# Optimization experiments

Measured on AMD Instinct MI355X. Metric: run time of the kernel, lower is better.

The kernel has to match this reference:

```python
import jax, jax.numpy as jnp
import numpy as np

B, S, H = 32, 1024, 768          # batch, seq_len, bert hidden
E, W, P = 128, 8, 512            # entities/sample, span width, rel pairs/sample
NT, NR = 5, 9                    # entity types, relation types
D1, HEADS1, D2, RD = 128, 2, 64, 32
REL_IN = 2 * D2 + RD + H         # 928


def _layernorm(x, g, b):
    m = x.mean(-1, keepdims=True)
    v = x.var(-1, keepdims=True)
    return (x - m) * jax.lax.rsqrt(v + 1e-5) * g + b


def _gat_dense(x, Wm, a_src, a_dst, bias, concat):
    # Fully-connected entity graph (incl. self-loops, PyG GATConv default).
    Bn, En, _ = x.shape
    Hh, D = a_src.shape
    h = (x @ Wm).reshape(Bn, En, Hh, D)                      # [B,E,h,D]
    s = jnp.einsum('behd,hd->beh', h, a_src)                 # source score
    d = jnp.einsum('behd,hd->beh', h, a_dst)                 # target score
    # edge j->i : e_ij = leaky_relu(s_j + d_i)
    e = jax.nn.leaky_relu(d[:, :, None, :] + s[:, None, :, :], 0.2)  # [B,i,j,h]
    alpha = jax.nn.softmax(e, axis=2)
    o = jnp.einsum('bijh,bjhd->bihd', alpha, h)
    o = o.reshape(Bn, En, Hh * D) if concat else o.mean(axis=2)
    return o + bias


def setup_inputs() -> dict:
    key = jax.random.key(0)
    ks = jax.random.split(key, 20)
    f = lambda k, shape: jax.random.normal(k, shape, jnp.float32) * 0.02
    return dict(
        sequence_output=jax.random.normal(ks[0], (B, S, H), jnp.float32),
        entity_starts=jax.random.randint(ks[1], (B, E), 0, S - W),
        entity_type_ids=jax.random.randint(ks[2], (B, E), 0, NT),
        pair_idx=jax.random.randint(ks[3], (B, P, 2), 0, E),
        rel_type_ids=jax.random.randint(ks[4], (B, P), 0, NR),
        entity_type_emb=f(ks[5], (NT, H)),
        rel_type_emb=f(ks[6], (NR, RD)),
        W1=f(ks[7], (H, HEADS1 * D1)), a_src1=f(ks[8], (HEADS1, D1)),
        a_dst1=f(ks[9], (HEADS1, D1)), b1=jnp.zeros((HEADS1 * D1,), jnp.float32),
        ln1_g=jnp.ones((HEADS1 * D1,), jnp.float32), ln1_b=jnp.zeros((HEADS1 * D1,), jnp.float32),
        W2=f(ks[10], (HEADS1 * D1, D2)), a_src2=f(ks[11], (1, D2)),
        a_dst2=f(ks[12], (1, D2)), b2=jnp.zeros((D2,), jnp.float32),
        ln2_g=jnp.ones((D2,), jnp.float32), ln2_b=jnp.zeros((D2,), jnp.float32),
        Wr1=f(ks[13], (REL_IN, 256)), br1=jnp.zeros((256,), jnp.float32),
        Wr2=f(ks[14], (256, 1)), br2=jnp.zeros((1,), jnp.float32),
    )


def reference(sequence_output, entity_starts, entity_type_ids, pair_idx, rel_type_ids,
              entity_type_emb, rel_type_emb,
              W1, a_src1, a_dst1, b1, ln1_g, ln1_b,
              W2, a_src2, a_dst2, b2, ln2_g, ln2_b,
              Wr1, br1, Wr2, br2):
    bidx = jnp.arange(B)[:, None]
    # --- per-entity attention pooling over span tokens ---
    tok_idx = entity_starts[:, :, None] + jnp.arange(W)            # [B,E,W]
    toks = sequence_output[jnp.arange(B)[:, None, None], tok_idx]  # [B,E,W,H]
    mean = toks.mean(axis=2)                                       # [B,E,H]
    attn = jax.nn.softmax(jnp.einsum('bewh,beh->bew', toks, mean), axis=-1)
    pooled = jnp.einsum('bew,bewh->beh', attn, toks)
    x = pooled + entity_type_emb[entity_type_ids]                  # [B,E,H]
    # --- 2-layer GAT over fully-connected entity graph ---
    x = jax.nn.elu(_layernorm(_gat_dense(x, W1, a_src1, a_dst1, b1, True), ln1_g, ln1_b))
    x = jax.nn.elu(_layernorm(_gat_dense(x, W2, a_src2, a_dst2, b2, False), ln2_g, ln2_b))
    # --- gather-concat relation MLP scoring ---
    cls = sequence_output[:, 0, :]                                 # [B,H]
    x1 = x[bidx, pair_idx[:, :, 0]]                                # [B,P,64]
    x2 = x[bidx, pair_idx[:, :, 1]]
    rel = rel_type_emb[rel_type_ids]                               # [B,P,32]
    pv = jnp.concatenate([x1, x2, rel, jnp.broadcast_to(cls[:, None, :], (B, P, H))], axis=-1)
    scores = (jax.nn.relu(pv @ Wr1 + br1) @ Wr2 + br2)[..., 0]     # [B,P]
    return scores
```

## Files before the change

kernel.cpp:

```cpp
#include <hip/hip_runtime.h>
#include <hip/hip_bf16.h>

#define BB 32
#define SS 1024
#define HHH 768
#define EE 128
#define WW 8
#define PP 512
#define RDD 32

typedef __attribute__((ext_vector_type(8))) short bf16x8;
typedef __attribute__((ext_vector_type(8))) unsigned short us8;
typedef __attribute__((ext_vector_type(4))) unsigned short us4;
typedef __attribute__((ext_vector_type(4))) float f32x4;

__device__ __forceinline__ unsigned short f2bf(float v) {
    __hip_bfloat16 h = __float2bfloat16(v);
    return *(unsigned short*)&h;
}
__device__ __forceinline__ float bf2f(unsigned short u) {
    unsigned int x = ((unsigned int)u) << 16;
    float f; __builtin_memcpy(&f, &x, 4);
    return f;
}

__global__ __launch_bounds__(256) void pool_prep_kernel(
    const float* __restrict__ seq, const int* __restrict__ starts,
    const int* __restrict__ types, const float* __restrict__ temb,
    unsigned short* __restrict__ xout,
    const float* __restrict__ W1, unsigned short* __restrict__ Wt,
    const float* __restrict__ Wr1, unsigned short* __restrict__ Wtr,
    const float* __restrict__ W2, unsigned short* __restrict__ W2t,
    const float* __restrict__ remb, unsigned short* __restrict__ rembb,
    float* __restrict__ basep) {
    int tid = threadIdx.x;
    __shared__ float sbuf[WW * HHH];
    __shared__ float scred[WW];
    __shared__ float attn_s[WW];

    if (blockIdx.x < BB * EE) {
        int be = blockIdx.x;
        int b = be >> 7;
        int start = starts[be];
        const float4* bp4 = (const float4*)(seq + ((size_t)b * SS + start) * HHH);
        for (int idx = tid; idx < WW * (HHH / 4); idx += 256) {
            int w = idx / (HHH / 4), h4 = idx % (HHH / 4);
            float4 v = bp4[(size_t)w * (HHH / 4) + h4];
            sbuf[w * HHH + h4 * 4 + 0] = v.x; sbuf[w * HHH + h4 * 4 + 1] = v.y;
            sbuf[w * HHH + h4 * 4 + 2] = v.z; sbuf[w * HHH + h4 * 4 + 3] = v.w;
        }
        __syncthreads();

        float sc[WW];
#pragma unroll
        for (int w = 0; w < WW; w++) sc[w] = 0.f;
#pragma unroll
        for (int c = 0; c < 3; c++) {
            int h = tid + 256 * c;
            float s = 0.f;
#pragma unroll
            for (int w = 0; w < WW; w++) s += sbuf[w * HHH + h];
            float m = s * (1.0f / WW);
#pragma unroll
            for (int w = 0; w < WW; w++) sc[w] += sbuf[w * HHH + h] * m;
        }
        if (tid < WW) scred[tid] = 0.f;
        __syncthreads();
        int lane = tid & 63;
#pragma unroll
        for (int w = 0; w < WW; w++) {
            float v = sc[w];
            for (int o = 32; o > 0; o >>= 1) v += __shfl_down(v, o, 64);
            if (lane == 0) atomicAdd(&scred[w], v);
        }
        __syncthreads();
        if (tid == 0) {
            float mx = scred[0];
            for (int w = 1; w < WW; w++) mx = fmaxf(mx, scred[w]);
            float ssum = 0.f;
            float a[WW];
            for (int w = 0; w < WW; w++) { a[w] = __expf(scred[w] - mx); ssum += a[w]; }
            float inv = 1.f / ssum;
            for (int w = 0; w < WW; w++) attn_s[w] = a[w] * inv;
        }
        __syncthreads();

        int t = types[be];
        const float* emb = temb + (size_t)t * HHH;
#pragma unroll
        for (int c = 0; c < 3; c++) {
            int h = tid + 256 * c;
            float p = 0.f;
#pragma unroll
            for (int w = 0; w < WW; w++) p += attn_s[w] * sbuf[w * HHH + h];
            xout[(size_t)be * HHH + h] = f2bf(p + emb[h]);
        }
        return;
    }

    int blk = blockIdx.x - BB * EE;
    if (blk < 48) {
        int k0 = blk * 16;
        for (int i = tid; i < 16 * 256; i += 256)
            sbuf[i] = W1[(size_t)(k0 + (i >> 8)) * 256 + (i & 255)];
        __syncthreads();
        int n = tid;
        us8 v0, v1;
#pragma unroll
        for (int kk = 0; kk < 8; kk++) v0[kk] = f2bf(sbuf[kk * 256 + n]);
#pragma unroll
        for (int kk = 0; kk < 8; kk++) v1[kk] = f2bf(sbuf[(8 + kk) * 256 + n]);
        *(us8*)(Wt + (size_t)n * HHH + k0) = v0;
        *(us8*)(Wt + (size_t)n * HHH + k0 + 8) = v1;
    } else if (blk < 58) {
        int k0 = (blk - 48) * 16;
        for (int i = tid; i < 16 * 256; i += 256)
            sbuf[i] = Wr1[(size_t)(k0 + (i >> 8)) * 256 + (i & 255)];
        __syncthreads();
        int n = tid;
        us8 v0, v1;
#pragma unroll
        for (int kk = 0; kk < 8; kk++) v0[kk] = f2bf(sbuf[kk * 256 + n]);
#pragma unroll
        for (int kk = 0; kk < 8; kk++) v1[kk] = f2bf(sbuf[(8 + kk) * 256 + n]);
        *(us8*)(Wtr + (size_t)n * 160 + k0) = v0;
        *(us8*)(Wtr + (size_t)n * 160 + k0 + 8) = v1;
    } else if (blk < 74) {
        int k0 = (blk - 58) * 16;
        for (int i = tid; i < 16 * 64; i += 256)
            sbuf[(i >> 6) * 64 + (i & 63)] = W2[(size_t)(k0 + (i >> 6)) * 64 + (i & 63)];
        __syncthreads();
        if (tid < 64) {
            int n = tid;
            us8 v0, v1;
#pragma unroll
            for (int kk = 0; kk < 8; kk++) v0[kk] = f2bf(sbuf[kk * 64 + n]);
#pragma unroll
            for (int kk = 0; kk < 8; kk++) v1[kk] = f2bf(sbuf[(8 + kk) * 64 + n]);
            *(us8*)(W2t + (size_t)n * 256 + k0) = v0;
            *(us8*)(W2t + (size_t)n * 256 + k0 + 8) = v1;
        }
    } else if (blk == 74) {
        for (int i = tid; i < 9 * RDD; i += 256) rembb[i] = f2bf(remb[i]);
    } else {
        int pc = blk - 75;
        int kc = pc % 12;
        int b = pc / 12;
        int n = tid;
        if (n < 64) sbuf[4096 + n] = seq[(size_t)b * SS * HHH + kc * 64 + n];
        __syncthreads();
        float acc = 0.f;
        const float* w = Wr1 + (size_t)(160 + kc * 64) * 256 + n;
#pragma unroll 16
        for (int k = 0; k < 64; k++) acc += sbuf[4096 + k] * w[(size_t)k * 256];
        basep[((size_t)kc * 32 + b) * 256 + n] = acc;
    }
}

__global__ __launch_bounds__(256) void gemm1_mfma_kernel(
    const unsigned short* __restrict__ Xb, const unsigned short* __restrict__ Wt,
    float* __restrict__ C) {
    const int K = HHH;
    int n0 = blockIdx.x * 64;
    int m0 = blockIdx.y * 64;
    int tid = threadIdx.x;
    int wave = tid >> 6, lane = tid & 63;
    int wm = (wave >> 1) * 32, wn = (wave & 1) * 32;

    __shared__ __align__(16) unsigned short As[64][40];
    __shared__ __align__(16) unsigned short Bs[64][40];

    f32x4 acc[2][2] = {};
    int ar = tid >> 2;
    int ac = (tid & 3) * 8;
    int fr = lane & 15;
    int fk = (lane >> 4) * 8;

    for (int k0 = 0; k0 < K; k0 += 32) {
        us8 av = *(const us8*)(Xb + (size_t)(m0 + ar) * K + k0 + ac);
        us8 bv = *(const us8*)(Wt + (size_t)(n0 + ar) * K + k0 + ac);
        *(us8*)(&As[ar][ac]) = av;
        *(us8*)(&Bs[ar][ac]) = bv;
        __syncthreads();

        bf16x8 a0 = *(const bf16x8*)(&As[wm + fr][fk]);
        bf16x8 a1 = *(const bf16x8*)(&As[wm + 16 + fr][fk]);
        bf16x8 b0 = *(const bf16x8*)(&Bs[wn + fr][fk]);
        bf16x8 b1 = *(const bf16x8*)(&Bs[wn + 16 + fr][fk]);

        acc[0][0] = __builtin_amdgcn_mfma_f32_16x16x32_bf16(a0, b0, acc[0][0], 0, 0, 0);
        acc[0][1] = __builtin_amdgcn_mfma_f32_16x16x32_bf16(a0, b1, acc[0][1], 0, 0, 0);
        acc[1][0] = __builtin_amdgcn_mfma_f32_16x16x32_bf16(a1, b0, acc[1][0], 0, 0, 0);
        acc[1][1] = __builtin_amdgcn_mfma_f32_16x16x32_bf16(a1, b1, acc[1][1], 0, 0, 0);
        __syncthreads();
    }

    int crow = (lane >> 4) * 4;
    int ccol = lane & 15;
#pragma unroll
    for (int mi = 0; mi < 2; mi++)
#pragma unroll
        for (int ni = 0; ni < 2; ni++)
#pragma unroll
            for (int r = 0; r < 4; r++)
                C[(size_t)(m0 + wm + mi * 16 + crow + r) * 256 +
                  n0 + wn + ni * 16 + ccol] = acc[mi][ni][r];
}

__global__ void sd1_kernel(const float* __restrict__ h1, const float* __restrict__ asrc,
                           const float* __restrict__ adst, float* __restrict__ s1,
                           float* __restrict__ d1) {
    int beh = blockIdx.x;
    int h = beh & 1;
    int be = beh >> 1;
    int lane = threadIdx.x;
    const float* row = h1 + (size_t)be * 256 + h * 128;
    float v0 = row[lane], v1 = row[lane + 64];
    float ss = v0 * asrc[h * 128 + lane] + v1 * asrc[h * 128 + lane + 64];
    float dd = v0 * adst[h * 128 + lane] + v1 * adst[h * 128 + lane + 64];
    for (int o = 32; o > 0; o >>= 1) {
        ss += __shfl_down(ss, o, 64);
        dd += __shfl_down(dd, o, 64);
    }
    if (lane == 0) { s1[beh] = ss; d1[beh] = dd; }
}

__global__ __launch_bounds__(256) void gat1_fused_kernel(
    const float* __restrict__ h1, const float* __restrict__ s1,
    const float* __restrict__ d1, const float* __restrict__ b1,
    const float* __restrict__ gamma, const float* __restrict__ beta,
    unsigned short* __restrict__ g1b) {
    int b = blockIdx.x >> 2;
    int c = blockIdx.x & 3;
    int tid = threadIdx.x;
    int wave = tid >> 6, lane = tid & 63;
    int h = wave >> 1, m = wave & 1;
    int fr = lane & 15;
    int fk = (lane >> 4) * 8;

    __shared__ __align__(16) unsigned short h1T[2][128][136];
    __shared__ float ssh[2][128];
    __shared__ float dsh[2][128];
    __shared__ float lnred[32][2][2];

    {
        const float4* src4 = (const float4*)(h1 + (size_t)b * 128 * 256);
        for (int it = 0; it < 32; it++) {
            int i4 = tid + it * 256;
            int j = i4 >> 6;
            int c4 = i4 & 63;
            float4 v = src4[(size_t)j * 64 + c4];
            int d = c4 * 4;
            int hh = d >> 7, dl = d & 127;
            h1T[hh][dl + 0][j] = f2bf(v.x);
            h1T[hh][dl + 1][j] = f2bf(v.y);
            h1T[hh][dl + 2][j] = f2bf(v.z);
            h1T[hh][dl + 3][j] = f2bf(v.w);
        }
        int hh = tid >> 7, j = tid & 127;
        ssh[hh][j] = s1[((size_t)b * 128 + j) * 2 + hh];
        dsh[hh][j] = d1[((size_t)b * 128 + j) * 2 + hh];
    }
    __syncthreads();

    bf16x8 afrag[4];
    {
        float dd = dsh[h][c * 32 + m * 16 + fr];
        float ev[4][8];
        float mx = -1e30f;
#pragma unroll
        for (int ks = 0; ks < 4; ks++)
#pragma unroll
            for (int jj = 0; jj < 8; jj++) {
                float e = dd + ssh[h][ks * 32 + fk + jj];
                e = e >= 0.f ? e : 0.2f * e;
                ev[ks][jj] = e;
                mx = fmaxf(mx, e);
            }
        mx = fmaxf(mx, __shfl_xor(mx, 16, 64));
        mx = fmaxf(mx, __shfl_xor(mx, 32, 64));
        float sm = 0.f;
#pragma unroll
        for (int ks = 0; ks < 4; ks++)
#pragma unroll
            for (int jj = 0; jj < 8; jj++) {
                float e = __expf(ev[ks][jj] - mx);
                ev[ks][jj] = e;
                sm += e;
            }
        sm += __shfl_xor(sm, 16, 64);
        sm += __shfl_xor(sm, 32, 64);
        float inv = 1.f / sm;
#pragma unroll
        for (int ks = 0; ks < 4; ks++) {
            bf16x8 a;
#pragma unroll
            for (int jj = 0; jj < 8; jj++)
                a[jj] = (short)f2bf(ev[ks][jj] * inv);
            afrag[ks] = a;
        }
    }

    f32x4 acc[8] = {};
#pragma unroll
    for (int ks = 0; ks < 4; ks++)
#pragma unroll
        for (int ni = 0; ni < 8; ni++) {
            bf16x8 bv = *(const bf16x8*)(&h1T[h][ni * 16 + fr][ks * 32 + fk]);
            acc[ni] = __builtin_amdgcn_mfma_f32_16x16x32_bf16(
                afrag[ks], bv, acc[ni], 0, 0, 0);
        }

    int crow = (lane >> 4) * 4;
    int ccol = lane & 15;
    float bv_[8], gv[8], bev[8];
#pragma unroll
    for (int ni = 0; ni < 8; ni++) {
        int d = h * 128 + ni * 16 + ccol;
        bv_[ni] = b1[d]; gv[ni] = gamma[d]; bev[ni] = beta[d];
    }
    float vv[4][8];
#pragma unroll
    for (int r = 0; r < 4; r++) {
        float s = 0.f, q = 0.f;
#pragma unroll
        for (int ni = 0; ni < 8; ni++) {
            float v = acc[ni][r] + bv_[ni];
            vv[r][ni] = v;
            s += v;
            q += v * v;
        }
        s += __shfl_xor(s, 1, 64); s += __shfl_xor(s, 2, 64);
        s += __shfl_xor(s, 4, 64); s += __shfl_xor(s, 8, 64);
        q += __shfl_xor(q, 1, 64); q += __shfl_xor(q, 2, 64);
        q += __shfl_xor(q, 4, 64); q += __shfl_xor(q, 8, 64);
        if ((lane & 15) == 0) {
            lnred[m * 16 + crow + r][h][0] = s;
            lnred[m * 16 + crow + r][h][1] = q;
        }
    }
    __syncthreads();
#pragma unroll
    for (int r = 0; r < 4; r++) {
        int row = m * 16 + crow + r;
        float s = lnred[row][0][0] + lnred[row][1][0];
        float q = lnred[row][0][1] + lnred[row][1][1];
        float mean = s * (1.f / 256.f);
        float var = q * (1.f / 256.f) - mean * mean;
        float rs = rsqrtf(var + 1e-5f);
        unsigned short* dst = g1b + (size_t)(b * 128 + c * 32 + row) * 256 + h * 128;
#pragma unroll
        for (int ni = 0; ni < 8; ni++) {
            float y = (vv[r][ni] - mean) * rs * gv[ni] + bev[ni];
            y = y > 0.f ? y : (__expf(y) - 1.f);
            dst[ni * 16 + ccol] = f2bf(y);
        }
    }
}

__global__ __launch_bounds__(256) void gemm2_mfma_kernel(
    const unsigned short* __restrict__ g1b, const unsigned short* __restrict__ W2t,
    const float* __restrict__ asrc, const float* __restrict__ adst,
    float* __restrict__ h2, float* __restrict__ s2, float* __restrict__ d2) {
    int m0 = blockIdx.x * 64;
    int tid = threadIdx.x;
    int wave = tid >> 6, lane = tid & 63;
    int wm = (wave >> 1) * 32, wn = (wave & 1) * 32;

    __shared__ __align__(16) unsigned short As[64][72];
    __shared__ __align__(16) unsigned short Bs[64][72];
    __shared__ float sdred[64][2][2];

    f32x4 acc[2][2] = {};
    int fr = lane & 15;
    int fk = (lane >> 4) * 8;

    for (int kc = 0; kc < 4; kc++) {
        for (int it = 0; it < 2; it++) {
            int i = tid + it * 256;
            int row = i >> 3, c = i & 7;
            *(us8*)(&As[row][c * 8]) =
                *(const us8*)(g1b + (size_t)(m0 + row) * 256 + kc * 64 + c * 8);
            *(us8*)(&Bs[row][c * 8]) =
                *(const us8*)(W2t + (size_t)row * 256 + kc * 64 + c * 8);
        }
        __syncthreads();
#pragma unroll
        for (int ks = 0; ks < 2; ks++) {
            int kb = ks * 32 + fk;
            bf16x8 a0 = *(const bf16x8*)(&As[wm + fr][kb]);
            bf16x8 a1 = *(const bf16x8*)(&As[wm + 16 + fr][kb]);
            bf16x8 b0 = *(const bf16x8*)(&Bs[wn + fr][kb]);
            bf16x8 b1 = *(const bf16x8*)(&Bs[wn + 16 + fr][kb]);
            acc[0][0] = __builtin_amdgcn_mfma_f32_16x16x32_bf16(a0, b0, acc[0][0], 0, 0, 0);
            acc[0][1] = __builtin_amdgcn_mfma_f32_16x16x32_bf16(a0, b1, acc[0][1], 0, 0, 0);
            acc[1][0] = __builtin_amdgcn_mfma_f32_16x16x32_bf16(a1, b0, acc[1][0], 0, 0, 0);
            acc[1][1] = __builtin_amdgcn_mfma_f32_16x16x32_bf16(a1, b1, acc[1][1], 0, 0, 0);
        }
        __syncthreads();
    }

    int crow = (lane >> 4) * 4;
    int ccol = lane & 15;
    float asv[2], adv[2];
#pragma unroll
    for (int ni = 0; ni < 2; ni++) {
        int n = wn + ni * 16 + ccol;
        asv[ni] = asrc[n];
        adv[ni] = adst[n];
    }
#pragma unroll
    for (int mi = 0; mi < 2; mi++) {
#pragma unroll
        for (int r = 0; r < 4; r++) {
            float sp = 0.f, dp = 0.f;
#pragma unroll
            for (int ni = 0; ni < 2; ni++) {
                float v = acc[mi][ni][r];
                h2[(size_t)(m0 + wm + mi * 16 + crow + r) * 64 +
                   wn + ni * 16 + ccol] = v;
                sp += v * asv[ni];
                dp += v * adv[ni];
            }
            for (int msk = 1; msk < 16; msk <<= 1) {
                sp += __shfl_xor(sp, msk, 64);
                dp += __shfl_xor(dp, msk, 64);
            }
            if ((lane & 15) == 0) {
                int row = wm + mi * 16 + crow + r;
                sdred[row][wn >> 5][0] = sp;
                sdred[row][wn >> 5][1] = dp;
            }
        }
    }
    __syncthreads();
    if (tid < 64 && wave == 0) {
        s2[m0 + tid] = sdred[tid][0][0] + sdred[tid][1][0];
        d2[m0 + tid] = sdred[tid][0][1] + sdred[tid][1][1];
    }
}

__global__ __launch_bounds__(256) void gat2_fused_kernel(
    const float* __restrict__ h2, const float* __restrict__ s2,
    const float* __restrict__ d2, const float* __restrict__ b2v,
    const float* __restrict__ gamma, const float* __restrict__ beta,
    unsigned short* __restrict__ x2b) {
    int b = blockIdx.x >> 1;
    int c = blockIdx.x & 1;
    int tid = threadIdx.x;
    int wave = tid >> 6, lane = tid & 63;
    int fr = lane & 15;
    int fk = (lane >> 4) * 8;

    __shared__ __align__(16) unsigned short h2T[64][136];
    __shared__ float ssh[128];
    __shared__ float dsh[128];

    {
        const float4* src4 = (const float4*)(h2 + (size_t)b * 128 * 64);
        for (int it = 0; it < 8; it++) {
            int i4 = tid + it * 256;
            int j = i4 >> 4;
            int c4 = i4 & 15;
            float4 v = src4[(size_t)j * 16 + c4];
            int d = c4 * 4;
            h2T[d + 0][j] = f2bf(v.x);
            h2T[d + 1][j] = f2bf(v.y);
            h2T[d + 2][j] = f2bf(v.z);
            h2T[d + 3][j] = f2bf(v.w);
        }
        if (tid < 128) ssh[tid] = s2[(size_t)b * 128 + tid];
        else dsh[tid - 128] = d2[(size_t)b * 128 + (tid - 128)];
    }
    __syncthreads();

    bf16x8 afrag[4];
    {
        float dd = dsh[c * 64 + wave * 16 + fr];
        float ev[4][8];
        float mx = -1e30f;
#pragma unroll
        for (int ks = 0; ks < 4; ks++)
#pragma unroll
            for (int jj = 0; jj < 8; jj++) {
                float e = dd + ssh[ks * 32 + fk + jj];
                e = e >= 0.f ? e : 0.2f * e;
                ev[ks][jj] = e;
                mx = fmaxf(mx, e);
            }
        mx = fmaxf(mx, __shfl_xor(mx, 16, 64));
        mx = fmaxf(mx, __shfl_xor(mx, 32, 64));
        float sm = 0.f;
#pragma unroll
        for (int ks = 0; ks < 4; ks++)
#pragma unroll
            for (int jj = 0; jj < 8; jj++) {
                float e = __expf(ev[ks][jj] - mx);
                ev[ks][jj] = e;
                sm += e;
            }
        sm += __shfl_xor(sm, 16, 64);
        sm += __shfl_xor(sm, 32, 64);
        float inv = 1.f / sm;
#pragma unroll
        for (int ks = 0; ks < 4; ks++) {
            bf16x8 a;
#pragma unroll
            for (int jj = 0; jj < 8; jj++)
                a[jj] = (short)f2bf(ev[ks][jj] * inv);
            afrag[ks] = a;
        }
    }

    f32x4 acc[4] = {};
#pragma unroll
    for (int ks = 0; ks < 4; ks++)
#pragma unroll
        for (int ni = 0; ni < 4; ni++) {
            bf16x8 bv = *(const bf16x8*)(&h2T[ni * 16 + fr][ks * 32 + fk]);
            acc[ni] = __builtin_amdgcn_mfma_f32_16x16x32_bf16(
                afrag[ks], bv, acc[ni], 0, 0, 0);
        }

    int crow = (lane >> 4) * 4;
    int ccol = lane & 15;
    float bv_[4], gv[4], bev[4];
#pragma unroll
    for (int ni = 0; ni < 4; ni++) {
        int d = ni * 16 + ccol;
        bv_[ni] = b2v[d]; gv[ni] = gamma[d]; bev[ni] = beta[d];
    }
#pragma unroll
    for (int r = 0; r < 4; r++) {
        float v[4];
        float s = 0.f;
#pragma unroll
        for (int ni = 0; ni < 4; ni++) {
            v[ni] = acc[ni][r] + bv_[ni];
            s += v[ni];
        }
        s += __shfl_xor(s, 1, 64); s += __shfl_xor(s, 2, 64);
        s += __shfl_xor(s, 4, 64); s += __shfl_xor(s, 8, 64);
        float mean = s * (1.f / 64.f);
        float sq = 0.f;
#pragma unroll
        for (int ni = 0; ni < 4; ni++) {
            float dv = v[ni] - mean;
            sq += dv * dv;
        }
        sq += __shfl_xor(sq, 1, 64); sq += __shfl_xor(sq, 2, 64);
        sq += __shfl_xor(sq, 4, 64); sq += __shfl_xor(sq, 8, 64);
        float rs = rsqrtf(sq * (1.f / 64.f) + 1e-5f);
        int i = c * 64 + wave * 16 + crow + r;
        unsigned short* dst = x2b + (size_t)(b * 128 + i) * 64;
#pragma unroll
        for (int ni = 0; ni < 4; ni++) {
            float y = (v[ni] - mean) * rs * gv[ni] + bev[ni];
            y = y > 0.f ? y : (__expf(y) - 1.f);
            dst[ni * 16 + ccol] = f2bf(y);
        }
    }
}

__global__ __launch_bounds__(256) void score_mfma_kernel(
    const unsigned short* __restrict__ x2b, const float* __restrict__ basep,
    const float* __restrict__ br1,
    const int* __restrict__ pair_idx, const int* __restrict__ rel_ids,
    const unsigned short* __restrict__ rembb, const unsigned short* __restrict__ Wtr,
    const float* __restrict__ Wr2, const float* __restrict__ br2,
    float* __restrict__ out) {
    int blk = blockIdx.x;
    int b = blk >> 3;
    int p0 = (blk & 7) * 64;
    int tid = threadIdx.x;
    int wave = tid >> 6, lane = tid & 63;
    int wn = wave * 64;

    __shared__ __align__(16) unsigned short As[64][168];
    __shared__ __align__(16) unsigned short Bs[256][40];
    __shared__ float sred[64][4];
    __shared__ int prs[64][3];

    if (tid < 64) {
        int p = p0 + tid;
        prs[tid][0] = pair_idx[((size_t)b * PP + p) * 2 + 0];
        prs[tid][1] = pair_idx[((size_t)b * PP + p) * 2 + 1];
        prs[tid][2] = rel_ids[(size_t)b * PP + p];
    }
    __syncthreads();
    for (int it = 0; it < 10; it++) {
        int idx = tid + it * 256;
        int m = idx / 40, c = idx % 40;
        int k0 = c * 4;
        us4 v;
        if (k0 < 64)
            v = *(const us4*)(x2b + ((size_t)b * EE + prs[m][0]) * 64 + k0);
        else if (k0 < 128)
            v = *(const us4*)(x2b + ((size_t)b * EE + prs[m][1]) * 64 + (k0 - 64));
        else
            v = *(const us4*)(rembb + prs[m][2] * RDD + (k0 - 128));
        *(us4*)(&As[m][k0]) = v;
    }

    f32x4 acc[4][4] = {};
    int fr = lane & 15;
    int fk = (lane >> 4) * 8;

    for (int kc = 0; kc < 5; kc++) {
        for (int it = 0; it < 4; it++) {
            int i = tid + it * 256;
            int n = i >> 2, c = i & 3;
            *(us8*)(&Bs[n][c * 8]) =
                *(const us8*)(Wtr + (size_t)n * 160 + kc * 32 + c * 8);
        }
        __syncthreads();
        bf16x8 a[4], bv[4];
#pragma unroll
        for (int mi = 0; mi < 4; mi++)
            a[mi] = *(const bf16x8*)(&As[mi * 16 + fr][kc * 32 + fk]);
#pragma unroll
        for (int ni = 0; ni < 4; ni++)
            bv[ni] = *(const bf16x8*)(&Bs[wn + ni * 16 + fr][fk]);
#pragma unroll
        for (int mi = 0; mi < 4; mi++)
#pragma unroll
            for (int ni = 0; ni < 4; ni++)
                acc[mi][ni] = __builtin_amdgcn_mfma_f32_16x16x32_bf16(
                    a[mi], bv[ni], acc[mi][ni], 0, 0, 0);
        __syncthreads();
    }

    int crow = (lane >> 4) * 4;
    int ccol = lane & 15;
    float basev[4], w2v[4];
#pragma unroll
    for (int ni = 0; ni < 4; ni++) {
        int n = wn + ni * 16 + ccol;
        float bb = br1[n];
#pragma unroll
        for (int kc = 0; kc < 12; kc++)
            bb += basep[((size_t)kc * 32 + b) * 256 + n];
        basev[ni] = bb;
        w2v[ni] = Wr2[n];
    }
#pragma unroll
    for (int mi = 0; mi < 4; mi++) {
#pragma unroll
        for (int r = 0; r < 4; r++) {
            float p = 0.f;
#pragma unroll
            for (int ni = 0; ni < 4; ni++)
                p += fmaxf(acc[mi][ni][r] + basev[ni], 0.f) * w2v[ni];
            for (int msk = 1; msk < 16; msk <<= 1)
                p += __shfl_xor(p, msk, 64);
            if ((lane & 15) == 0)
                sred[mi * 16 + crow + r][wave] = p;
        }
    }
    __syncthreads();
    if (tid < 64) {
        float s = sred[tid][0] + sred[tid][1] + sred[tid][2] + sred[tid][3] + br2[0];
        out[(size_t)b * PP + p0 + tid] = s;
    }
}

extern "C" void kernel_launch(void* const* d_in, const int* in_sizes, int n_in,
                              void* d_out, int out_size, void* d_ws, size_t ws_size,
                              hipStream_t stream) {
    (void)in_sizes; (void)n_in; (void)out_size; (void)ws_size;
    const float* seq      = (const float*)d_in[0];
    const int*   starts   = (const int*)d_in[1];
    const int*   types    = (const int*)d_in[2];
    const int*   pair_idx = (const int*)d_in[3];
    const int*   rel_ids  = (const int*)d_in[4];
    const float* temb     = (const float*)d_in[5];
    const float* remb     = (const float*)d_in[6];
    const float* W1       = (const float*)d_in[7];
    const float* a_src1   = (const float*)d_in[8];
    const float* a_dst1   = (const float*)d_in[9];
    const float* b1       = (const float*)d_in[10];
    const float* ln1_g    = (const float*)d_in[11];
    const float* ln1_b    = (const float*)d_in[12];
    const float* W2       = (const float*)d_in[13];
    const float* a_src2   = (const float*)d_in[14];
    const float* a_dst2   = (const float*)d_in[15];
    const float* b2       = (const float*)d_in[16];
    const float* ln2_g    = (const float*)d_in[17];
    const float* ln2_b    = (const float*)d_in[18];
    const float* Wr1      = (const float*)d_in[19];
    const float* br1      = (const float*)d_in[20];
    const float* Wr2      = (const float*)d_in[21];
    const float* br2      = (const float*)d_in[22];
    float* out = (float*)d_out;

    unsigned short* xb    = (unsigned short*)d_ws;
    unsigned short* Wt    = xb + (size_t)4096 * 768;
    unsigned short* Wtr   = Wt + (size_t)256 * 768;
    unsigned short* W2t   = Wtr + (size_t)256 * 160;
    unsigned short* rembb = W2t + (size_t)64 * 256;
    unsigned short* g1b   = rembb + 512;
    unsigned short* x2b   = g1b + (size_t)4096 * 256;
    float* fbase = (float*)(x2b + (size_t)4096 * 64);
    float* h1    = fbase;
    float* s1    = h1 + (size_t)4096 * 256;
    float* d1    = s1 + 8192;
    float* h2    = d1 + 8192;
    float* s2    = h2 + (size_t)4096 * 64;
    float* d2    = s2 + 4096;
    float* basep = d2 + 4096;

    pool_prep_kernel<<<BB * EE + 75 + 12 * 32, 256, 0, stream>>>(
        seq, starts, types, temb, xb, W1, Wt, Wr1, Wtr, W2, W2t, remb, rembb, basep);
    gemm1_mfma_kernel<<<dim3(4, 64), 256, 0, stream>>>(xb, Wt, h1);
    sd1_kernel<<<BB * EE * 2, 64, 0, stream>>>(h1, a_src1, a_dst1, s1, d1);
    gat1_fused_kernel<<<BB * 4, 256, 0, stream>>>(h1, s1, d1, b1, ln1_g, ln1_b, g1b);
    gemm2_mfma_kernel<<<64, 256, 0, stream>>>(g1b, W2t, a_src2, a_dst2, h2, s2, d2);
    gat2_fused_kernel<<<BB * 2, 256, 0, stream>>>(h2, s2, d2, b2, ln2_g, ln2_b, x2b);
    score_mfma_kernel<<<BB * PP / 64, 256, 0, stream>>>(x2b, basep, br1, pair_idx,
                                                        rel_ids, rembb, Wtr, Wr2,
                                                        br2, out);
}
```

Measured before the change: 245.8 us.

## Fuse GAT score reductions and layer-2 GEMM into neighbouring kernels with bf16 transposed intermediates

The GEMM1 epilogue now computes the per-head source and destination attention partial sums and writes h1 as transposed bf16, which removes the separate sd1 kernel and the fp32 h1 round trip. The layer-1 GAT kernel now also performs the W2 projection and the s2/d2 reductions, removing the standalone gemm2 kernel and the g1b buffer. GAT2 reads a pre-transposed bf16 h2. This cuts two launches and intermediate memory traffic. In exchange it adds more shared memory in the fused kernel and reads W2 directly from global memory inside it.

New measurement: 228.9 us. 6.9% less time.

```diff
diff --git a/kernel.cpp b/kernel.cpp
--- a/kernel.cpp
+++ b/kernel.cpp
@@ -17,11 +17,6 @@
 __device__ __forceinline__ unsigned short f2bf(float v) {
     __hip_bfloat16 h = __float2bfloat16(v);
     return *(unsigned short*)&h;
-}
-__device__ __forceinline__ float bf2f(unsigned short u) {
-    unsigned int x = ((unsigned int)u) << 16;
-    float f; __builtin_memcpy(&f, &x, 4);
-    return f;
 }
 
 __global__ __launch_bounds__(256) void pool_prep_kernel(
@@ -159,7 +154,9 @@
 
 __global__ __launch_bounds__(256) void gemm1_mfma_kernel(
     const unsigned short* __restrict__ Xb, const unsigned short* __restrict__ Wt,
-    float* __restrict__ C) {
+    const float* __restrict__ asrc1, const float* __restrict__ adst1,
+    unsigned short* __restrict__ h1Tg,
+    float* __restrict__ ps_s, float* __restrict__ ps_d) {
     const int K = HHH;
     int n0 = blockIdx.x * 64;
     int m0 = blockIdx.y * 64;
@@ -169,6 +166,8 @@
 
     __shared__ __align__(16) unsigned short As[64][40];
     __shared__ __align__(16) unsigned short Bs[64][40];
+    __shared__ __align__(16) unsigned short T[64][72];
+    __shared__ float sdred[64][2][2];
 
     f32x4 acc[2][2] = {};
     int ar = tid >> 2;
@@ -197,218 +196,18 @@
 
     int crow = (lane >> 4) * 4;
     int ccol = lane & 15;
-#pragma unroll
-    for (int mi = 0; mi < 2; mi++)
-#pragma unroll
-        for (int ni = 0; ni < 2; ni++)
-#pragma unroll
-            for (int r = 0; r < 4; r++)
-                C[(size_t)(m0 + wm + mi * 16 + crow + r) * 256 +
-                  n0 + wn + ni * 16 + ccol] = acc[mi][ni][r];
-}
-
-__global__ void sd1_kernel(const float* __restrict__ h1, const float* __restrict__ asrc,
-                           const float* __restrict__ adst, float* __restrict__ s1,
-                           float* __restrict__ d1) {
-    int beh = blockIdx.x;
-    int h = beh & 1;
-    int be = beh >> 1;
-    int lane = threadIdx.x;
-    const float* row = h1 + (size_t)be * 256 + h * 128;
-    float v0 = row[lane], v1 = row[lane + 64];
-    float ss = v0 * asrc[h * 128 + lane] + v1 * asrc[h * 128 + lane + 64];
-    float dd = v0 * adst[h * 128 + lane] + v1 * adst[h * 128 + lane + 64];
-    for (int o = 32; o > 0; o >>= 1) {
-        ss += __shfl_down(ss, o, 64);
-        dd += __shfl_down(dd, o, 64);
-    }
-    if (lane == 0) { s1[beh] = ss; d1[beh] = dd; }
-}
-
-__global__ __launch_bounds__(256) void gat1_fused_kernel(
-    const float* __restrict__ h1, const float* __restrict__ s1,
-    const float* __restrict__ d1, const float* __restrict__ b1,
-    const float* __restrict__ gamma, const float* __restrict__ beta,
-    unsigned short* __restrict__ g1b) {
-    int b = blockIdx.x >> 2;
-    int c = blockIdx.x & 3;
-    int tid = threadIdx.x;
-    int wave = tid >> 6, lane = tid & 63;
-    int h = wave >> 1, m = wave & 1;
-    int fr = lane & 15;
-    int fk = (lane >> 4) * 8;
-
-    __shared__ __align__(16) unsigned short h1T[2][128][136];
-    __shared__ float ssh[2][128];
-    __shared__ float dsh[2][128];
-    __shared__ float lnred[32][2][2];
-
-    {
-        const float4* src4 = (const float4*)(h1 + (size_t)b * 128 * 256);
-        for (int it = 0; it < 32; it++) {
-            int i4 = tid + it * 256;
-            int j = i4 >> 6;
-            int c4 = i4 & 63;
-            float4 v = src4[(size_t)j * 64 + c4];
-            int d = c4 * 4;
-            int hh = d >> 7, dl = d & 127;
-            h1T[hh][dl + 0][j] = f2bf(v.x);
-            h1T[hh][dl + 1][j] = f2bf(v.y);
-            h1T[hh][dl + 2][j] = f2bf(v.z);
-            h1T[hh][dl + 3][j] = f2bf(v.w);
-        }
-        int hh = tid >> 7, j = tid & 127;
-        ssh[hh][j] = s1[((size_t)b * 128 + j) * 2 + hh];
-        dsh[hh][j] = d1[((size_t)b * 128 + j) * 2 + hh];
-    }
-    __syncthreads();
-
-    bf16x8 afrag[4];
-    {
-        float dd = dsh[h][c * 32 + m * 16 + fr];
-        float ev[4][8];
-        float mx = -1e30f;
-#pragma unroll
-        for (int ks = 0; ks < 4; ks++)
-#pragma unroll
-            for (int jj = 0; jj < 8; jj++) {
-                float e = dd + ssh[h][ks * 32 + fk + jj];
-                e = e >= 0.f ? e : 0.2f * e;
-                ev[ks][jj] = e;
-                mx = fmaxf(mx, e);
-            }
-        mx = fmaxf(mx, __shfl_xor(mx, 16, 64));
-        mx = fmaxf(mx, __shfl_xor(mx, 32, 64));
-        float sm = 0.f;
-#pragma unroll
-        for (int ks = 0; ks < 4; ks++)
-#pragma unroll
-            for (int jj = 0; jj < 8; jj++) {
-                float e = __expf(ev[ks][jj] - mx);
-                ev[ks][jj] = e;
-                sm += e;
-            }
-        sm += __shfl_xor(sm, 16, 64);
-        sm += __shfl_xor(sm, 32, 64);
-        float inv = 1.f / sm;
-#pragma unroll
-        for (int ks = 0; ks < 4; ks++) {
-            bf16x8 a;
-#pragma unroll
-            for (int jj = 0; jj < 8; jj++)
-                a[jj] = (short)f2bf(ev[ks][jj] * inv);
-            afrag[ks] = a;
-        }
-    }
-
-    f32x4 acc[8] = {};
-#pragma unroll
-    for (int ks = 0; ks < 4; ks++)
-#pragma unroll
-        for (int ni = 0; ni < 8; ni++) {
-            bf16x8 bv = *(const bf16x8*)(&h1T[h][ni * 16 + fr][ks * 32 + fk]);
-            acc[ni] = __builtin_amdgcn_mfma_f32_16x16x32_bf16(
-                afrag[ks], bv, acc[ni], 0, 0, 0);
-        }
-
-    int crow = (lane >> 4) * 4;
-    int ccol = lane & 15;
-    float bv_[8], gv[8], bev[8];
-#pragma unroll
-    for (int ni = 0; ni < 8; ni++) {
-        int d = h * 128 + ni * 16 + ccol;
-        bv_[ni] = b1[d]; gv[ni] = gamma[d]; bev[ni] = beta[d];
-    }
-    float vv[4][8];
-#pragma unroll
-    for (int r = 0; r < 4; r++) {
-        float s = 0.f, q = 0.f;
-#pragma unroll
-        for (int ni = 0; ni < 8; ni++) {
-            float v = acc[ni][r] + bv_[ni];
-            vv[r][ni] = v;
-            s += v;
-            q += v * v;
-        }
-        s += __shfl_xor(s, 1, 64); s += __shfl_xor(s, 2, 64);
-        s += __shfl_xor(s, 4, 64); s += __shfl_xor(s, 8, 64);
-        q += __shfl_xor(q, 1, 64); q += __shfl_xor(q, 2, 64);
-        q += __shfl_xor(q, 4, 64); q += __shfl_xor(q, 8, 64);
-        if ((lane & 15) == 0) {
-            lnred[m * 16 + crow + r][h][0] = s;
-            lnred[m * 16 + crow + r][h][1] = q;
-        }
-    }
-    __syncthreads();
-#pragma unroll
-    for (int r = 0; r < 4; r++) {
-        int row = m * 16 + crow + r;
-        float s = lnred[row][0][0] + lnred[row][1][0];
-        float q = lnred[row][0][1] + lnred[row][1][1];
-        float mean = s * (1.f / 256.f);
-        float var = q * (1.f / 256.f) - mean * mean;
-        float rs = rsqrtf(var + 1e-5f);
-        unsigned short* dst = g1b + (size_t)(b * 128 + c * 32 + row) * 256 + h * 128;
-#pragma unroll
-        for (int ni = 0; ni < 8; ni++) {
-            float y = (vv[r][ni] - mean) * rs * gv[ni] + bev[ni];
-            y = y > 0.f ? y : (__expf(y) - 1.f);
-            dst[ni * 16 + ccol] = f2bf(y);
-        }
-    }
-}
-
-__global__ __launch_bounds__(256) void gemm2_mfma_kernel(
-    const unsigned short* __restrict__ g1b, const unsigned short* __restrict__ W2t,
-    const float* __restrict__ asrc, const float* __restrict__ adst,
-    float* __restrict__ h2, float* __restrict__ s2, float* __restrict__ d2) {
-    int m0 = blockIdx.x * 64;
-    int tid = threadIdx.x;
-    int wave = tid >> 6, lane = tid & 63;
-    int wm = (wave >> 1) * 32, wn = (wave & 1) * 32;
-
-    __shared__ __align__(16) unsigned short As[64][72];
-    __shared__ __align__(16) unsigned short Bs[64][72];
-    __shared__ float sdred[64][2][2];
-
-    f32x4 acc[2][2] = {};
-    int fr = lane & 15;
-    int fk = (lane >> 4) * 8;
-
-    for (int kc = 0; kc < 4; kc++) {
-        for (int it = 0; it < 2; it++) {
-            int i = tid + it * 256;
-            int row = i >> 3, c = i & 7;
-            *(us8*)(&As[row][c * 8]) =
-                *(const us8*)(g1b + (size_t)(m0 + row) * 256 + kc * 64 + c * 8);
-            *(us8*)(&Bs[row][c * 8]) =
-                *(const us8*)(W2t + (size_t)row * 256 + kc * 64 + c * 8);
-        }
-        __syncthreads();
-#pragma unroll
-        for (int ks = 0; ks < 2; ks++) {
-            int kb = ks * 32 + fk;
-            bf16x8 a0 = *(const bf16x8*)(&As[wm + fr][kb]);
-            bf16x8 a1 = *(const bf16x8*)(&As[wm + 16 + fr][kb]);
-            bf16x8 b0 = *(const bf16x8*)(&Bs[wn + fr][kb]);
-            bf16x8 b1 = *(const bf16x8*)(&Bs[wn + 16 + fr][kb]);
-            acc[0][0] = __builtin_amdgcn_mfma_f32_16x16x32_bf16(a0, b0, acc[0][0], 0, 0, 0);
-            acc[0][1] = __builtin_amdgcn_mfma_f32_16x16x32_bf16(a0, b1, acc[0][1], 0, 0, 0);
-            acc[1][0] = __builtin_amdgcn_mfma_f32_16x16x32_bf16(a1, b0, acc[1][0], 0, 0, 0);
-            acc[1][1] = __builtin_amdgcn_mfma_f32_16x16x32_bf16(a1, b1, acc[1][1], 0, 0, 0);
-        }
-        __syncthreads();
-    }
-
-    int crow = (lane >> 4) * 4;
-    int ccol = lane & 15;
+    int h = n0 >> 7;
+    int nb = (n0 >> 6) & 1;
+    int dbase = (n0 & 127) + wn;
+
     float asv[2], adv[2];
 #pragma unroll
     for (int ni = 0; ni < 2; ni++) {
-        int n = wn + ni * 16 + ccol;
-        asv[ni] = asrc[n];
-        adv[ni] = adst[n];
-    }
+        int d = dbase + ni * 16 + ccol;
+        asv[ni] = asrc1[h * 128 + d];
+        adv[ni] = adst1[h * 128 + d];
+    }
+
 #pragma unroll
     for (int mi = 0; mi < 2; mi++) {
 #pragma unroll
@@ -417,8 +216,7 @@
 #pragma unroll
             for (int ni = 0; ni < 2; ni++) {
                 float v = acc[mi][ni][r];
-                h2[(size_t)(m0 + wm + mi * 16 + crow + r) * 64 +
-                   wn + ni * 16 + ccol] = v;
+                T[wn + ni * 16 + ccol][wm + mi * 16 + crow + r] = f2bf(v);
                 sp += v * asv[ni];
                 dp += v * adv[ni];
             }
@@ -434,14 +232,215 @@
         }
     }
     __syncthreads();
-    if (tid < 64 && wave == 0) {
-        s2[m0 + tid] = sdred[tid][0][0] + sdred[tid][1][0];
-        d2[m0 + tid] = sdred[tid][0][1] + sdred[tid][1][1];
+
+    int b = m0 >> 7;
+    int j0 = m0 & 127;
+    if (tid < 64) {
+        float spt = sdred[tid][0][0] + sdred[tid][1][0];
+        float dpt = sdred[tid][0][1] + sdred[tid][1][1];
+        size_t o = (size_t)nb * 8192 + ((size_t)(m0 + tid)) * 2 + h;
+        ps_s[o] = spt;
+        ps_d[o] = dpt;
+    }
+    {
+        int d_l = tid >> 2, q = tid & 3;
+        us8 v0 = *(const us8*)(&T[d_l][q * 16]);
+        us8 v1 = *(const us8*)(&T[d_l][q * 16 + 8]);
+        size_t go = ((size_t)(b * 2 + h) * 128 + (n0 & 127) + d_l) * 128 + j0 + q * 16;
+        *(us8*)(h1Tg + go) = v0;
+        *(us8*)(h1Tg + go + 8) = v1;
     }
 }
 
+__global__ __launch_bounds__(256) void gat1_gemm2_kernel(
+    const unsigned short* __restrict__ h1Tg,
+    const float* __restrict__ ps_s, const float* __restrict__ ps_d,
+    const float* __restrict__ b1, const float* __restrict__ gamma,
+    const float* __restrict__ beta,
+    const unsigned short* __restrict__ W2t,
+    const float* __restrict__ asrc2, const float* __restrict__ adst2,
+    unsigned short* __restrict__ h2Tg, float* __restrict__ s2,
+    float* __restrict__ d2) {
+    int b = blockIdx.x >> 2;
+    int c = blockIdx.x & 3;
+    int tid = threadIdx.x;
+    int wave = tid >> 6, lane = tid & 63;
+    int h = wave >> 1, m = wave & 1;
+    int fr = lane & 15;
+    int fk = (lane >> 4) * 8;
+
+    __shared__ __align__(16) unsigned short h1T[2][128][136];
+    __shared__ float ssh[2][128];
+    __shared__ float dsh[2][128];
+    __shared__ float lnred[32][2][2];
+    __shared__ __align__(16) unsigned short g1s[32][264];
+    __shared__ float sdr2[32][2][2];
+    __shared__ __align__(16) unsigned short t2[64][40];
+
+    {
+        const us8* src = (const us8*)(h1Tg + (size_t)b * 32768);
+#pragma unroll
+        for (int it = 0; it < 16; it++) {
+            int i8 = tid + it * 256;
+            int row = i8 >> 4;
+            int j8 = i8 & 15;
+            *(us8*)(&h1T[row >> 7][row & 127][j8 * 8]) = src[i8];
+        }
+        int hh = tid >> 7, j = tid & 127;
+        size_t o = ((size_t)b * 128 + j) * 2 + hh;
+        ssh[hh][j] = ps_s[o] + ps_s[o + 8192];
+        dsh[hh][j] = ps_d[o] + ps_d[o + 8192];
+    }
+    __syncthreads();
+
+    bf16x8 afrag[4];
+    {
+        float dd = dsh[h][c * 32 + m * 16 + fr];
+        float ev[4][8];
+        float mx = -1e30f;
+#pragma unroll
+        for (int ks = 0; ks < 4; ks++)
+#pragma unroll
+            for (int jj = 0; jj < 8; jj++) {
+                float e = dd + ssh[h][ks * 32 + fk + jj];
+                e = e >= 0.f ? e : 0.2f * e;
+                ev[ks][jj] = e;
+                mx = fmaxf(mx, e);
+            }
+        mx = fmaxf(mx, __shfl_xor(mx, 16, 64));
+        mx = fmaxf(mx, __shfl_xor(mx, 32, 64));
+        float sm = 0.f;
+#pragma unroll
+        for (int ks = 0; ks < 4; ks++)
+#pragma unroll
+            for (int jj = 0; jj < 8; jj++) {
+                float e = __expf(ev[ks][jj] - mx);
+                ev[ks][jj] = e;
+                sm += e;
+            }
+        sm += __shfl_xor(sm, 16, 64);
+        sm += __shfl_xor(sm, 32, 64);
+        float inv = 1.f / sm;
+#pragma unroll
+        for (int ks = 0; ks < 4; ks++) {
+            bf16x8 a;
+#pragma unroll
+            for (int jj = 0; jj < 8; jj++)
+                a[jj] = (short)f2bf(ev[ks][jj] * inv);
+            afrag[ks] = a;
+        }
+    }
+
+    f32x4 acc[8] = {};
+#pragma unroll
+    for (int ks = 0; ks < 4; ks++)
+#pragma unroll
+        for (int ni = 0; ni < 8; ni++) {
+            bf16x8 bv = *(const bf16x8*)(&h1T[h][ni * 16 + fr][ks * 32 + fk]);
+            acc[ni] = __builtin_amdgcn_mfma_f32_16x16x32_bf16(
+                afrag[ks], bv, acc[ni], 0, 0, 0);
+        }
+
+    int crow = (lane >> 4) * 4;
+    int ccol = lane & 15;
+    float bv_[8], gv[8], bev[8];
+#pragma unroll
+    for (int ni = 0; ni < 8; ni++) {
+        int d = h * 128 + ni * 16 + ccol;
+        bv_[ni] = b1[d]; gv[ni] = gamma[d]; bev[ni] = beta[d];
+    }
+    float vv[4][8];
+#pragma unroll
+    for (int r = 0; r < 4; r++) {
+        float s = 0.f, q = 0.f;
+#pragma unroll
+        for (int ni = 0; ni < 8; ni++) {
+            float v = acc[ni][r] + bv_[ni];
+            vv[r][ni] = v;
+            s += v;
+            q += v * v;
+        }
+        s += __shfl_xor(s, 1, 64); s += __shfl_xor(s, 2, 64);
+        s += __shfl_xor(s, 4, 64); s += __shfl_xor(s, 8, 64);
+        q += __shfl_xor(q, 1, 64); q += __shfl_xor(q, 2, 64);
+        q += __shfl_xor(q, 4, 64); q += __shfl_xor(q, 8, 64);
+        if ((lane & 15) == 0) {
+            lnred[m * 16 + crow + r][h][0] = s;
+            lnred[m * 16 + crow + r][h][1] = q;
+        }
+    }
+    __syncthreads();
+#pragma unroll
+    for (int r = 0; r < 4; r++) {
+        int row = m * 16 + crow + r;
+        float s = lnred[row][0][0] + lnred[row][1][0];
+        float q = lnred[row][0][1] + lnred[row][1][1];
+        float mean = s * (1.f / 256.f);
+        float var = q * (1.f / 256.f) - mean * mean;
+        float rs = rsqrtf(var + 1e-5f);
+#pragma unroll
+        for (int ni = 0; ni < 8; ni++) {
+            float y = (vv[r][ni] - mean) * rs * gv[ni] + bev[ni];
+            y = y > 0.f ? y : (__expf(y) - 1.f);
+            g1s[row][h * 128 + ni * 16 + ccol] = f2bf(y);
+        }
+    }
+    __syncthreads();
+
+    int m2 = wave & 1;
+    int nb = wave >> 1;
+    f32x4 acc2[2] = {};
+#pragma unroll
+    for (int kc = 0; kc < 8; kc++) {
+        bf16x8 a = *(const bf16x8*)(&g1s[m2 * 16 + fr][kc * 32 + fk]);
+#pragma unroll
+        for (int ni = 0; ni < 2; ni++) {
+            bf16x8 wv = *(const bf16x8*)(W2t + (size_t)(nb * 32 + ni * 16 + fr) * 256 +
+                                         kc * 32 + fk);
+            acc2[ni] = __builtin_amdgcn_mfma_f32_16x16x32_bf16(a, wv, acc2[ni], 0, 0, 0);
+        }
+    }
+    float as2[2], ad2[2];
+#pragma unroll
+    for (int ni = 0; ni < 2; ni++) {
+        int n = nb * 32 + ni * 16 + ccol;
+        as2[ni] = asrc2[n];
+        ad2[ni] = adst2[n];
+    }
+#pragma unroll
+    for (int r = 0; r < 4; r++) {
+        int rl = m2 * 16 + crow + r;
+        float sp = 0.f, dp = 0.f;
+#pragma unroll
+        for (int ni = 0; ni < 2; ni++) {
+            float v = acc2[ni][r];
+            t2[nb * 32 + ni * 16 + ccol][rl] = f2bf(v);
+            sp += v * as2[ni];
+            dp += v * ad2[ni];
+        }
+        for (int msk = 1; msk < 16; msk <<= 1) {
+            sp += __shfl_xor(sp, msk, 64);
+            dp += __shfl_xor(dp, msk, 64);
+        }
+        if ((lane & 15) == 0) {
+            sdr2[rl][nb][0] = sp;
+            sdr2[rl][nb][1] = dp;
+        }
+    }
+    __syncthreads();
+    if (tid < 32) {
+        s2[(size_t)b * 128 + c * 32 + tid] = sdr2[tid][0][0] + sdr2[tid][1][0];
+        d2[(size_t)b * 128 + c * 32 + tid] = sdr2[tid][0][1] + sdr2[tid][1][1];
+    }
+    {
+        int d = tid >> 2, q = tid & 3;
+        us8 v = *(const us8*)(&t2[d][q * 8]);
+        *(us8*)(h2Tg + ((size_t)b * 64 + d) * 128 + c * 32 + q * 8) = v;
+    }
+}
+
 __global__ __launch_bounds__(256) void gat2_fused_kernel(
-    const float* __restrict__ h2, const float* __restrict__ s2,
+    const unsigned short* __restrict__ h2Tg, const float* __restrict__ s2,
     const float* __restrict__ d2, const float* __restrict__ b2v,
     const float* __restrict__ gamma, const float* __restrict__ beta,
     unsigned short* __restrict__ x2b) {
@@ -457,17 +456,13 @@
     __shared__ float dsh[128];
 
     {
-        const float4* src4 = (const float4*)(h2 + (size_t)b * 128 * 64);
-        for (int it = 0; it < 8; it++) {
-            int i4 = tid + it * 256;
-            int j = i4 >> 4;
-            int c4 = i4 & 15;
-            float4 v = src4[(size_t)j * 16 + c4];
-            int d = c4 * 4;
-            h2T[d + 0][j] = f2bf(v.x);
-            h2T[d + 1][j] = f2bf(v.y);
-            h2T[d + 2][j] = f2bf(v.z);
-            h2T[d + 3][j] = f2bf(v.w);
+        const us8* src = (const us8*)(h2Tg + (size_t)b * 64 * 128);
+#pragma unroll
+        for (int it = 0; it < 4; it++) {
+            int i8 = tid + it * 256;
+            int row = i8 >> 4;
+            int j8 = i8 & 15;
+            *(us8*)(&h2T[row][j8 * 8]) = src[i8];
         }
         if (tid < 128) ssh[tid] = s2[(size_t)b * 128 + tid];
         else dsh[tid - 128] = d2[(size_t)b * 128 + (tid - 128)];
@@ -698,24 +693,23 @@
     unsigned short* Wtr   = Wt + (size_t)256 * 768;
     unsigned short* W2t   = Wtr + (size_t)256 * 160;
     unsigned short* rembb = W2t + (size_t)64 * 256;
-    unsigned short* g1b   = rembb + 512;
-    unsigned short* x2b   = g1b + (size_t)4096 * 256;
+    unsigned short* h1Tg  = rembb + 512;
+    unsigned short* h2Tg  = h1Tg + (size_t)4096 * 256;
+    unsigned short* x2b   = h2Tg + (size_t)32 * 64 * 128;
     float* fbase = (float*)(x2b + (size_t)4096 * 64);
-    float* h1    = fbase;
-    float* s1    = h1 + (size_t)4096 * 256;
-    float* d1    = s1 + 8192;
-    float* h2    = d1 + 8192;
-    float* s2    = h2 + (size_t)4096 * 64;
+    float* ps_s  = fbase;
+    float* ps_d  = ps_s + 2 * 8192;
+    float* s2    = ps_d + 2 * 8192;
     float* d2    = s2 + 4096;
     float* basep = d2 + 4096;
 
     pool_prep_kernel<<<BB * EE + 75 + 12 * 32, 256, 0, stream>>>(
         seq, starts, types, temb, xb, W1, Wt, Wr1, Wtr, W2, W2t, remb, rembb, basep);
-    gemm1_mfma_kernel<<<dim3(4, 64), 256, 0, stream>>>(xb, Wt, h1);
-    sd1_kernel<<<BB * EE * 2, 64, 0, stream>>>(h1, a_src1, a_dst1, s1, d1);
-    gat1_fused_kernel<<<BB * 4, 256, 0, stream>>>(h1, s1, d1, b1, ln1_g, ln1_b, g1b);
-    gemm2_mfma_kernel<<<64, 256, 0, stream>>>(g1b, W2t, a_src2, a_dst2, h2, s2, d2);
-    gat2_fused_kernel<<<BB * 2, 256, 0, stream>>>(h2, s2, d2, b2, ln2_g, ln2_b, x2b);
+    gemm1_mfma_kernel<<<dim3(4, 64), 256, 0, stream>>>(xb, Wt, a_src1, a_dst1,
+                                                       h1Tg, ps_s, ps_d);
+    gat1_gemm2_kernel<<<BB * 4, 256, 0, stream>>>(h1Tg, ps_s, ps_d, b1, ln1_g, ln1_b,
+                                                  W2t, a_src2, a_dst2, h2Tg, s2, d2);
+    gat2_fused_kernel<<<BB * 2, 256, 0, stream>>>(h2Tg, s2, d2, b2, ln2_g, ln2_b, x2b);
     score_mfma_kernel<<<BB * PP / 64, 256, 0, stream>>>(x2b, basep, br1, pair_idx,
                                                         rel_ids, rembb, Wtr, Wr2,
                                                         br2, out);
```
